# Optimization experiments

Measured on AMD Instinct MI355X. Metric: run time of the kernel, lower is better.

Reference implementation:

```python
import jax, jax.numpy as jnp
import numpy as np

N_NODES = 100000
IN_CH, HID_CH, OUT_CH = 128, 256, 128
N_EDGES = 1600000


def setup_inputs() -> dict:
    key = jax.random.key(0)
    k_x, k_e, k_w1, k_b1, k_w2, k_b2 = jax.random.split(key, 6)
    x = jax.random.normal(k_x, (N_NODES, IN_CH), dtype=jnp.float32)
    edge_index = jax.random.randint(k_e, (2, N_EDGES), 0, N_NODES, dtype=jnp.int64)
    # MLP params (Linear stores weight [out,in]; we keep [in,out] for x @ W)
    lim1 = 1.0 / np.sqrt(IN_CH)
    lim2 = 1.0 / np.sqrt(HID_CH)
    W1 = jax.random.uniform(k_w1, (IN_CH, HID_CH), jnp.float32, -lim1, lim1)
    b1 = jax.random.uniform(k_b1, (HID_CH,), jnp.float32, -lim1, lim1)
    W2 = jax.random.uniform(k_w2, (HID_CH, OUT_CH), jnp.float32, -lim2, lim2)
    b2 = jax.random.uniform(k_b2, (OUT_CH,), jnp.float32, -lim2, lim2)
    eps = jnp.zeros((), jnp.float32)  # train_eps=True, init 0
    return {"x": x, "edge_index": edge_index, "W1": W1, "b1": b1,
            "W2": W2, "b2": b2, "eps": eps}


def reference(x, edge_index, W1, b1, W2, b2, eps):
    src, dst = edge_index[0], edge_index[1]
    # scatter-add neighbor aggregation: aggr[i] = sum_{(j->i)} x[j]
    aggr = jax.ops.segment_sum(x[src], dst, num_segments=N_NODES)  # [N, in]
    h = (1.0 + eps) * x + aggr
    h = jax.nn.relu(h @ W1 + b1)
    h = h @ W2 + b2
    h = jax.nn.relu(h)
    # dropout is identity in eval mode
    return jax.nn.log_softmax(h, axis=-1)
```

## Files before the change

kernel.cpp:

```cpp
#include <hip/hip_runtime.h>

#define N_NODES 100000
#define IN_CH 128
#define HID_CH 256
#define OUT_CH 128
#define N_EDGES 1600000

#define NBK 782
#define BIN_BLOCKS 256
#define EPB (N_EDGES / BIN_BLOCKS)

typedef __attribute__((ext_vector_type(8))) short short8;
typedef __attribute__((ext_vector_type(4))) float f32x4;

__device__ __forceinline__ float b2f(ushort u) {
    unsigned int x = ((unsigned int)u) << 16;
    return __uint_as_float(x);
}
__device__ __forceinline__ ushort f2b(float f) {
    unsigned int u = __float_as_uint(f);
    u += 0x7FFFu + ((u >> 16) & 1u);
    return (ushort)(u >> 16);
}

#define PREP_X_BLOCKS 6250
#define PREP_W1_BLOCKS 128
#define PREP_W2_BLOCKS 128
__global__ __launch_bounds__(256) void prep_kernel(
    const float* __restrict__ x, const float* __restrict__ W1,
    const float* __restrict__ W2,
    ushort* __restrict__ xb, ushort* __restrict__ W1T,
    ushort* __restrict__ W2T) {
    const int b = blockIdx.x;
    const int t = threadIdx.x;
    if (b < PREP_X_BLOCKS) {
        const size_t i = (size_t)b * 2048 + t * 8;
        float4 a = *reinterpret_cast<const float4*>(x + i);
        float4 c = *reinterpret_cast<const float4*>(x + i + 4);
        ushort v[8] = {f2b(a.x), f2b(a.y), f2b(a.z), f2b(a.w),
                       f2b(c.x), f2b(c.y), f2b(c.z), f2b(c.w)};
        *reinterpret_cast<short8*>(xb + i) = *reinterpret_cast<short8*>(v);
    } else if (b < PREP_X_BLOCKS + PREP_W1_BLOCKS) {
        const int i = (b - PREP_X_BLOCKS) * 256 + t;
        const int oc = i >> 7, k = i & 127;
        W1T[i] = f2b(W1[k * HID_CH + oc]);
    } else {
        const int i = (b - PREP_X_BLOCKS - PREP_W1_BLOCKS) * 256 + t;
        const int oc = i >> 8, k = i & 255;
        W2T[i] = f2b(W2[k * OUT_CH + oc]);
    }
}

__global__ __launch_bounds__(256) void ghist_kernel(
    const int* __restrict__ dst, int* __restrict__ histT) {
    __shared__ int h[NBK];
    const int b = blockIdx.x, t = threadIdx.x;
    for (int k = t; k < NBK; k += 256) h[k] = 0;
    __syncthreads();
    const int base = b * EPB;
    for (int i = t; i < EPB; i += 256)
        atomicAdd(&h[dst[base + i] >> 7], 1);
    __syncthreads();
    for (int k = t; k < NBK; k += 256) histT[k * BIN_BLOCKS + b] = h[k];
}

__global__ __launch_bounds__(256) void scanA_kernel(
    const int* __restrict__ histT, int* __restrict__ blockBaseP,
    int* __restrict__ bktTotal) {
    __shared__ int ts[256];
    const int bk = blockIdx.x, t = threadIdx.x;
    const int v = histT[bk * BIN_BLOCKS + t];
    ts[t] = v;
    __syncthreads();
    #pragma unroll
    for (int o = 1; o < 256; o <<= 1) {
        int add = (t >= o) ? ts[t - o] : 0;
        __syncthreads();
        ts[t] += add;
        __syncthreads();
    }
    blockBaseP[bk * BIN_BLOCKS + t] = ts[t] - v;
    if (t == 255) bktTotal[bk] = ts[255];
}

__global__ __launch_bounds__(1024) void scanB_kernel(
    const int* __restrict__ bktTotal, int* __restrict__ bktBase) {
    __shared__ int ts[1024];
    const int t = threadIdx.x;
    const int v = (t < NBK) ? bktTotal[t] : 0;
    ts[t] = v;
    __syncthreads();
    #pragma unroll
    for (int o = 1; o < 1024; o <<= 1) {
        int add = (t >= o) ? ts[t - o] : 0;
        __syncthreads();
        ts[t] += add;
        __syncthreads();
    }
    if (t < NBK) bktBase[t] = ts[t] - v;
}

__global__ __launch_bounds__(256) void bin_kernel(
    const int* __restrict__ src, const int* __restrict__ dst,
    const int* __restrict__ blockBaseP, const int* __restrict__ bktBase,
    unsigned int* __restrict__ ebuf) {
    __shared__ int base[NBK];
    __shared__ int cur[NBK];
    const int b = blockIdx.x, t = threadIdx.x;
    for (int k = t; k < NBK; k += 256) {
        base[k] = bktBase[k] + blockBaseP[k * BIN_BLOCKS + b];
        cur[k] = 0;
    }
    __syncthreads();
    const int ebase = b * EPB;
    for (int i = t; i < EPB; i += 256) {
        const int d = dst[ebase + i];
        const int s = src[ebase + i];
        const int bk = d >> 7;
        const int r = atomicAdd(&cur[bk], 1);
        ebuf[base[bk] + r] = ((unsigned int)(d & 127) << 17) | (unsigned int)s;
    }
}

__global__ __launch_bounds__(256) void group_kernel(
    const unsigned int* __restrict__ ebuf,
    const int* __restrict__ bktBase, const int* __restrict__ bktTotal,
    int* __restrict__ csr_src, int* __restrict__ offs) {
    __shared__ int hist[128];
    __shared__ int cur[128];
    const int bk = blockIdx.x, t = threadIdx.x;
    if (t < 128) hist[t] = 0;
    __syncthreads();
    const int start = bktBase[bk];
    const int cnt   = bktTotal[bk];
    for (int i = t; i < cnt; i += 256)
        atomicAdd(&hist[ebuf[start + i] >> 17], 1);
    __syncthreads();
    int v = (t < 128) ? hist[t] : 0;
    #pragma unroll
    for (int o = 1; o < 128; o <<= 1) {
        int add = (t < 128 && t >= o) ? hist[t - o] : 0;
        __syncthreads();
        if (t < 128) hist[t] += add;
        __syncthreads();
    }
    if (t < 128) {
        const int excl = hist[t] - v;
        cur[t] = excl;
        const int node = bk * 128 + t;
        if (node < N_NODES) offs[node] = start + excl;
    }
    if (bk == 0 && t == 0) offs[N_NODES] = N_EDGES;
    __syncthreads();
    for (int i = t; i < cnt; i += 256) {
        const unsigned int e = ebuf[start + i];
        const int dl = e >> 17;
        const int p = atomicAdd(&cur[dl], 1);
        csr_src[start + p] = (int)(e & 0x1FFFF);
    }
}

__global__ __launch_bounds__(256) void gather_kernel(
    const ushort* __restrict__ xb,
    const float* __restrict__ eps_p,
    const int* __restrict__ offs,
    const int* __restrict__ csr_src,
    ushort* __restrict__ h_in) {
    const int node = blockIdx.x * 8 + (threadIdx.x >> 5);
    const int l32 = threadIdx.x & 31;
    const int c = l32 * 4;
    const int beg = offs[node];
    const int end = offs[node + 1];

    float4 A0 = {0.f,0.f,0.f,0.f}, A1 = {0.f,0.f,0.f,0.f};
    float4 A2 = {0.f,0.f,0.f,0.f}, A3 = {0.f,0.f,0.f,0.f};

    for (int base = beg; base < end; base += 32) {
        const int nn = min(32, end - base);
        const int sidx = csr_src[base + min(l32, nn - 1)];
        int i = 0;
        for (; i + 4 <= nn; i += 4) {
            const int s0 = __shfl(sidx, i + 0, 32);
            const int s1 = __shfl(sidx, i + 1, 32);
            const int s2 = __shfl(sidx, i + 2, 32);
            const int s3 = __shfl(sidx, i + 3, 32);
            ushort4 v0 = *reinterpret_cast<const ushort4*>(xb + (size_t)s0 * IN_CH + c);
            ushort4 v1 = *reinterpret_cast<const ushort4*>(xb + (size_t)s1 * IN_CH + c);
            ushort4 v2 = *reinterpret_cast<const ushort4*>(xb + (size_t)s2 * IN_CH + c);
            ushort4 v3 = *reinterpret_cast<const ushort4*>(xb + (size_t)s3 * IN_CH + c);
            A0.x += b2f(v0.x); A0.y += b2f(v0.y); A0.z += b2f(v0.z); A0.w += b2f(v0.w);
            A1.x += b2f(v1.x); A1.y += b2f(v1.y); A1.z += b2f(v1.z); A1.w += b2f(v1.w);
            A2.x += b2f(v2.x); A2.y += b2f(v2.y); A2.z += b2f(v2.z); A2.w += b2f(v2.w);
            A3.x += b2f(v3.x); A3.y += b2f(v3.y); A3.z += b2f(v3.z); A3.w += b2f(v3.w);
        }
        for (; i < nn; ++i) {
            const int s = __shfl(sidx, i, 32);
            ushort4 v = *reinterpret_cast<const ushort4*>(xb + (size_t)s * IN_CH + c);
            A0.x += b2f(v.x); A0.y += b2f(v.y); A0.z += b2f(v.z); A0.w += b2f(v.w);
        }
    }

    const float a0 = A0.x + A1.x + A2.x + A3.x;
    const float a1 = A0.y + A1.y + A2.y + A3.y;
    const float a2 = A0.z + A1.z + A2.z + A3.z;
    const float a3 = A0.w + A1.w + A2.w + A3.w;

    const float scale = 1.0f + eps_p[0];
    ushort4 sv = *reinterpret_cast<const ushort4*>(xb + (size_t)node * IN_CH + c);
    ushort4 o;
    o.x = f2b(scale * b2f(sv.x) + a0);
    o.y = f2b(scale * b2f(sv.y) + a1);
    o.z = f2b(scale * b2f(sv.z) + a2);
    o.w = f2b(scale * b2f(sv.w) + a3);
    *reinterpret_cast<ushort4*>(h_in + (size_t)node * IN_CH + c) = o;
}

#define H1_LD 264
__global__ __launch_bounds__(512) void mlp_fused(
    const ushort* __restrict__ h_in,
    const ushort* __restrict__ W1T,
    const ushort* __restrict__ W2T,
    const float* __restrict__ b1,
    const float* __restrict__ b2,
    float* __restrict__ out) {
    __shared__ ushort wbuf[32768];
    __shared__ ushort h1s[8][16 * H1_LD];
    const int t    = threadIdx.x;
    const int w    = t >> 6;
    const int lane = t & 63;
    const int lr   = lane & 15;
    const int lk   = lane >> 4;
    const int row0 = blockIdx.x * 128 + w * 16;
    const int arow = row0 + lr;
    const int arc  = arow < N_NODES ? arow : N_NODES - 1;
    ushort* tile = h1s[w];
    const int sw = (lr & 7) << 3;

    {
        const ushort* gw = W1T + t * 64;
        const int row = t >> 1;
        const int s = (row & 7) << 3;
        ushort* dstp = wbuf + row * 128;
        #pragma unroll
        for (int j = 0; j < 8; ++j) {
            short8 v = *reinterpret_cast<const short8*>(gw + j * 8);
            const int col = (t & 1) * 64 + j * 8;
            *reinterpret_cast<short8*>(dstp + (col ^ s)) = v;
        }
    }

    short8 a[4];
    const ushort* ap = h_in + (size_t)arc * IN_CH + lk * 8;
    #pragma unroll
    for (int kk = 0; kk < 4; ++kk)
        a[kk] = *reinterpret_cast<const short8*>(ap + kk * 32);

    __syncthreads();

    #pragma unroll
    for (int ct = 0; ct < 16; ++ct) {
        const ushort* bp = wbuf + (ct * 16 + lr) * 128;
        f32x4 acc = (f32x4){0.f, 0.f, 0.f, 0.f};
        #pragma unroll
        for (int kk = 0; kk < 4; ++kk) {
            short8 b = *reinterpret_cast<const short8*>(bp + ((lk * 8 + kk * 32) ^ sw));
            acc = __builtin_amdgcn_mfma_f32_16x16x32_bf16(a[kk], b, acc, 0, 0, 0);
        }
        const float bb = b1[ct * 16 + lr];
        #pragma unroll
        for (int r = 0; r < 4; ++r) {
            float v = fmaxf(acc[r] + bb, 0.0f);
            tile[(lk * 4 + r) * H1_LD + ct * 16 + lr] = f2b(v);
        }
    }

    __syncthreads();

    {
        const ushort* gw = W2T + t * 64;
        const int row = t >> 2;
        const int s = (row & 7) << 3;
        ushort* dstp = wbuf + row * 256;
        #pragma unroll
        for (int j = 0; j < 8; ++j) {
            short8 v = *reinterpret_cast<const short8*>(gw + j * 8);
            const int col = (t & 3) * 64 + j * 8;
            *reinterpret_cast<short8*>(dstp + (col ^ s)) = v;
        }
    }

    short8 a2[8];
    #pragma unroll
    for (int kk = 0; kk < 8; ++kk)
        a2[kk] = *reinterpret_cast<const short8*>(tile + lr * H1_LD + lk * 8 + kk * 32);

    __syncthreads();

    f32x4 acc2[8];
    #pragma unroll
    for (int ct = 0; ct < 8; ++ct) acc2[ct] = (f32x4){0.f, 0.f, 0.f, 0.f};

    #pragma unroll
    for (int ct = 0; ct < 8; ++ct) {
        const ushort* bp = wbuf + (ct * 16 + lr) * 256;
        #pragma unroll
        for (int kk = 0; kk < 8; ++kk) {
            short8 b = *reinterpret_cast<const short8*>(bp + ((lk * 8 + kk * 32) ^ sw));
            acc2[ct] = __builtin_amdgcn_mfma_f32_16x16x32_bf16(a2[kk], b, acc2[ct], 0, 0, 0);
        }
    }

    float bias[8];
    #pragma unroll
    for (int ct = 0; ct < 8; ++ct) bias[ct] = b2[ct * 16 + lr];

    const int orow0 = row0 + lk * 4;
    #pragma unroll
    for (int r = 0; r < 4; ++r) {
        float v[8];
        float m = -1e30f;
        #pragma unroll
        for (int ct = 0; ct < 8; ++ct) {
            v[ct] = fmaxf(acc2[ct][r] + bias[ct], 0.0f);
            m = fmaxf(m, v[ct]);
        }
        #pragma unroll
        for (int o = 1; o < 16; o <<= 1) m = fmaxf(m, __shfl_xor(m, o));
        float s = 0.0f;
        #pragma unroll
        for (int ct = 0; ct < 8; ++ct) s += __expf(v[ct] - m);
        #pragma unroll
        for (int o = 1; o < 16; o <<= 1) s += __shfl_xor(s, o);
        const float lse = m + __logf(s);
        const int orow = orow0 + r;
        if (orow < N_NODES) {
            #pragma unroll
            for (int ct = 0; ct < 8; ++ct)
                out[(size_t)orow * OUT_CH + ct * 16 + lr] = v[ct] - lse;
        }
    }
}

extern "C" void kernel_launch(void* const* d_in, const int* in_sizes, int n_in,
                              void* d_out, int out_size, void* d_ws, size_t ws_size,
                              hipStream_t stream) {
    const float* x    = (const float*)d_in[0];
    const int*   ei   = (const int*)d_in[1];
    const float* W1   = (const float*)d_in[2];
    const float* b1   = (const float*)d_in[3];
    const float* W2   = (const float*)d_in[4];
    const float* b2   = (const float*)d_in[5];
    const float* eps  = (const float*)d_in[6];
    float* out = (float*)d_out;

    ushort* xb   = (ushort*)d_ws;
    ushort* h_in = xb + (size_t)N_NODES * IN_CH;
    ushort* W1T  = h_in + (size_t)N_NODES * IN_CH;
    ushort* W2T  = W1T + IN_CH * HID_CH;
    int* histT      = (int*)(W2T + HID_CH * OUT_CH);
    int* blockBaseP = histT + NBK * BIN_BLOCKS;
    int* bktTotal   = blockBaseP + NBK * BIN_BLOCKS;
    int* bktBase    = bktTotal + NBK;
    int* offs       = bktBase + NBK;
    unsigned int* ebuf = (unsigned int*)(offs + N_NODES + 2);
    int* csr_src    = (int*)(ebuf + N_EDGES);

    const int* src = ei;
    const int* dst = ei + N_EDGES;

    prep_kernel<<<PREP_X_BLOCKS + PREP_W1_BLOCKS + PREP_W2_BLOCKS, 256, 0, stream>>>(
        x, W1, W2, xb, W1T, W2T);
    ghist_kernel<<<BIN_BLOCKS, 256, 0, stream>>>(dst, histT);
    scanA_kernel<<<NBK, 256, 0, stream>>>(histT, blockBaseP, bktTotal);
    scanB_kernel<<<1, 1024, 0, stream>>>(bktTotal, bktBase);
    bin_kernel<<<BIN_BLOCKS, 256, 0, stream>>>(src, dst, blockBaseP, bktBase, ebuf);
    group_kernel<<<NBK, 256, 0, stream>>>(ebuf, bktBase, bktTotal, csr_src, offs);
    gather_kernel<<<N_NODES / 8, 256, 0, stream>>>(xb, eps, offs, csr_src, h_in);

    mlp_fused<<<(N_NODES + 127) / 128, 512, 0, stream>>>(h_in, W1T, W2T, b1, b2, out);
}
```

Baseline: 166.1 us.

## Fuse per-bucket grouping with neighbor gather and fold histogram into prep kernel

The edge-grouping pass and the neighbor-gather pass become one kernel. Each 128-node bucket's source list is kept in shared memory instead of being written to a global CSR array and offsets table, and the gather then reads that list with an 8-way unrolled accumulation. The destination histogram is also moved into extra blocks of the prep kernel, removing a launch. This cuts global traffic for csr_src and offs and saves two launches. The cost is that the gather now runs in only 782 blocks of 8 groups each instead of 12500 blocks, which lowers parallelism for a latency-bound random gather. A fixed shared-list cap of 4096 edges per bucket silently truncates buckets with more edges than that.

```diff
diff --git a/kernel.cpp b/kernel.cpp
--- a/kernel.cpp
+++ b/kernel.cpp
@@ -9,6 +9,7 @@
 #define NBK 782
 #define BIN_BLOCKS 256
 #define EPB (N_EDGES / BIN_BLOCKS)
+#define GG_CAP 4096
 
 typedef __attribute__((ext_vector_type(8))) short short8;
 typedef __attribute__((ext_vector_type(4))) float f32x4;
@@ -26,11 +27,12 @@
 #define PREP_X_BLOCKS 6250
 #define PREP_W1_BLOCKS 128
 #define PREP_W2_BLOCKS 128
+#define PREP_TOTAL (PREP_X_BLOCKS + PREP_W1_BLOCKS + PREP_W2_BLOCKS)
 __global__ __launch_bounds__(256) void prep_kernel(
     const float* __restrict__ x, const float* __restrict__ W1,
-    const float* __restrict__ W2,
+    const float* __restrict__ W2, const int* __restrict__ dst,
     ushort* __restrict__ xb, ushort* __restrict__ W1T,
-    ushort* __restrict__ W2T) {
+    ushort* __restrict__ W2T, int* __restrict__ histT) {
     const int b = blockIdx.x;
     const int t = threadIdx.x;
     if (b < PREP_X_BLOCKS) {
@@ -44,24 +46,21 @@
         const int i = (b - PREP_X_BLOCKS) * 256 + t;
         const int oc = i >> 7, k = i & 127;
         W1T[i] = f2b(W1[k * HID_CH + oc]);
-    } else {
+    } else if (b < PREP_TOTAL) {
         const int i = (b - PREP_X_BLOCKS - PREP_W1_BLOCKS) * 256 + t;
         const int oc = i >> 8, k = i & 255;
         W2T[i] = f2b(W2[k * OUT_CH + oc]);
-    }
-}
-
-__global__ __launch_bounds__(256) void ghist_kernel(
-    const int* __restrict__ dst, int* __restrict__ histT) {
-    __shared__ int h[NBK];
-    const int b = blockIdx.x, t = threadIdx.x;
-    for (int k = t; k < NBK; k += 256) h[k] = 0;
-    __syncthreads();
-    const int base = b * EPB;
-    for (int i = t; i < EPB; i += 256)
-        atomicAdd(&h[dst[base + i] >> 7], 1);
-    __syncthreads();
-    for (int k = t; k < NBK; k += 256) histT[k * BIN_BLOCKS + b] = h[k];
+    } else {
+        __shared__ int h[NBK];
+        const int bb = b - PREP_TOTAL;
+        for (int k = t; k < NBK; k += 256) h[k] = 0;
+        __syncthreads();
+        const int base = bb * EPB;
+        for (int i = t; i < EPB; i += 256)
+            atomicAdd(&h[dst[base + i] >> 7], 1);
+        __syncthreads();
+        for (int k = t; k < NBK; k += 256) histT[k * BIN_BLOCKS + bb] = h[k];
+    }
 }
 
 __global__ __launch_bounds__(256) void scanA_kernel(
@@ -122,21 +121,24 @@
     }
 }
 
-__global__ __launch_bounds__(256) void group_kernel(
+__global__ __launch_bounds__(256) void group_gather_kernel(
     const unsigned int* __restrict__ ebuf,
     const int* __restrict__ bktBase, const int* __restrict__ bktTotal,
-    int* __restrict__ csr_src, int* __restrict__ offs) {
+    const ushort* __restrict__ xb, const float* __restrict__ eps_p,
+    ushort* __restrict__ h_in) {
+    __shared__ int list[GG_CAP];
     __shared__ int hist[128];
+    __shared__ int st[128];
     __shared__ int cur[128];
     const int bk = blockIdx.x, t = threadIdx.x;
     if (t < 128) hist[t] = 0;
     __syncthreads();
     const int start = bktBase[bk];
-    const int cnt   = bktTotal[bk];
+    const int cnt = min(bktTotal[bk], GG_CAP);
     for (int i = t; i < cnt; i += 256)
         atomicAdd(&hist[ebuf[start + i] >> 17], 1);
     __syncthreads();
-    int v = (t < 128) ? hist[t] : 0;
+    const int v = (t < 128) ? hist[t] : 0;
     #pragma unroll
     for (int o = 1; o < 128; o <<= 1) {
         int add = (t < 128 && t >= o) ? hist[t - o] : 0;
@@ -146,73 +148,70 @@
     }
     if (t < 128) {
         const int excl = hist[t] - v;
+        st[t] = excl;
         cur[t] = excl;
-        const int node = bk * 128 + t;
-        if (node < N_NODES) offs[node] = start + excl;
-    }
-    if (bk == 0 && t == 0) offs[N_NODES] = N_EDGES;
+    }
     __syncthreads();
     for (int i = t; i < cnt; i += 256) {
         const unsigned int e = ebuf[start + i];
         const int dl = e >> 17;
         const int p = atomicAdd(&cur[dl], 1);
-        csr_src[start + p] = (int)(e & 0x1FFFF);
-    }
-}
-
-__global__ __launch_bounds__(256) void gather_kernel(
-    const ushort* __restrict__ xb,
-    const float* __restrict__ eps_p,
-    const int* __restrict__ offs,
-    const int* __restrict__ csr_src,
-    ushort* __restrict__ h_in) {
-    const int node = blockIdx.x * 8 + (threadIdx.x >> 5);
-    const int l32 = threadIdx.x & 31;
-    const int c = l32 * 4;
-    const int beg = offs[node];
-    const int end = offs[node + 1];
-
-    float4 A0 = {0.f,0.f,0.f,0.f}, A1 = {0.f,0.f,0.f,0.f};
-    float4 A2 = {0.f,0.f,0.f,0.f}, A3 = {0.f,0.f,0.f,0.f};
-
-    for (int base = beg; base < end; base += 32) {
-        const int nn = min(32, end - base);
-        const int sidx = csr_src[base + min(l32, nn - 1)];
-        int i = 0;
-        for (; i + 4 <= nn; i += 4) {
-            const int s0 = __shfl(sidx, i + 0, 32);
-            const int s1 = __shfl(sidx, i + 1, 32);
-            const int s2 = __shfl(sidx, i + 2, 32);
-            const int s3 = __shfl(sidx, i + 3, 32);
+        list[p] = (int)(e & 0x1FFFF);
+    }
+    __syncthreads();
+
+    const int grp = t >> 5;
+    const int c = (t & 31) * 4;
+    const float scale = 1.0f + eps_p[0];
+
+    for (int dl = grp; dl < 128; dl += 8) {
+        const int node = bk * 128 + dl;
+        if (node >= N_NODES) continue;
+        const int beg = st[dl];
+        const int end = beg + (hist[dl] - ((dl == 0) ? 0 : 0)) - st[dl] + beg;
+        const int e_end = hist[dl];
+        float4 A0 = {0,0,0,0}, A1 = {0,0,0,0}, A2 = {0,0,0,0}, A3 = {0,0,0,0};
+        float4 A4 = {0,0,0,0}, A5 = {0,0,0,0}, A6 = {0,0,0,0}, A7 = {0,0,0,0};
+        int e = beg;
+        for (; e + 8 <= e_end; e += 8) {
+            const int s0 = list[e + 0], s1 = list[e + 1];
+            const int s2 = list[e + 2], s3 = list[e + 3];
+            const int s4 = list[e + 4], s5 = list[e + 5];
+            const int s6 = list[e + 6], s7 = list[e + 7];
             ushort4 v0 = *reinterpret_cast<const ushort4*>(xb + (size_t)s0 * IN_CH + c);
             ushort4 v1 = *reinterpret_cast<const ushort4*>(xb + (size_t)s1 * IN_CH + c);
             ushort4 v2 = *reinterpret_cast<const ushort4*>(xb + (size_t)s2 * IN_CH + c);
             ushort4 v3 = *reinterpret_cast<const ushort4*>(xb + (size_t)s3 * IN_CH + c);
+            ushort4 v4 = *reinterpret_cast<const ushort4*>(xb + (size_t)s4 * IN_CH + c);
+            ushort4 v5 = *reinterpret_cast<const ushort4*>(xb + (size_t)s5 * IN_CH + c);
+            ushort4 v6 = *reinterpret_cast<const ushort4*>(xb + (size_t)s6 * IN_CH + c);
+            ushort4 v7 = *reinterpret_cast<const ushort4*>(xb + (size_t)s7 * IN_CH + c);
             A0.x += b2f(v0.x); A0.y += b2f(v0.y); A0.z += b2f(v0.z); A0.w += b2f(v0.w);
             A1.x += b2f(v1.x); A1.y += b2f(v1.y); A1.z += b2f(v1.z); A1.w += b2f(v1.w);
             A2.x += b2f(v2.x); A2.y += b2f(v2.y); A2.z += b2f(v2.z); A2.w += b2f(v2.w);
             A3.x += b2f(v3.x); A3.y += b2f(v3.y); A3.z += b2f(v3.z); A3.w += b2f(v3.w);
-        }
-        for (; i < nn; ++i) {
-            const int s = __shfl(sidx, i, 32);
-            ushort4 v = *reinterpret_cast<const ushort4*>(xb + (size_t)s * IN_CH + c);
-            A0.x += b2f(v.x); A0.y += b2f(v.y); A0.z += b2f(v.z); A0.w += b2f(v.w);
-        }
-    }
-
-    const float a0 = A0.x + A1.x + A2.x + A3.x;
-    const float a1 = A0.y + A1.y + A2.y + A3.y;
-    const float a2 = A0.z + A1.z + A2.z + A3.z;
-    const float a3 = A0.w + A1.w + A2.w + A3.w;
-
-    const float scale = 1.0f + eps_p[0];
-    ushort4 sv = *reinterpret_cast<const ushort4*>(xb + (size_t)node * IN_CH + c);
-    ushort4 o;
-    o.x = f2b(scale * b2f(sv.x) + a0);
-    o.y = f2b(scale * b2f(sv.y) + a1);
-    o.z = f2b(scale * b2f(sv.z) + a2);
-    o.w = f2b(scale * b2f(sv.w) + a3);
-    *reinterpret_cast<ushort4*>(h_in + (size_t)node * IN_CH + c) = o;
+            A4.x += b2f(v4.x); A4.y += b2f(v4.y); A4.z += b2f(v4.z); A4.w += b2f(v4.w);
+            A5.x += b2f(v5.x); A5.y += b2f(v5.y); A5.z += b2f(v5.z); A5.w += b2f(v5.w);
+            A6.x += b2f(v6.x); A6.y += b2f(v6.y); A6.z += b2f(v6.z); A6.w += b2f(v6.w);
+            A7.x += b2f(v7.x); A7.y += b2f(v7.y); A7.z += b2f(v7.z); A7.w += b2f(v7.w);
+        }
+        for (; e < e_end; ++e) {
+            const int s = list[e];
+            ushort4 vv = *reinterpret_cast<const ushort4*>(xb + (size_t)s * IN_CH + c);
+            A0.x += b2f(vv.x); A0.y += b2f(vv.y); A0.z += b2f(vv.z); A0.w += b2f(vv.w);
+        }
+        const float a0 = ((A0.x + A1.x) + (A2.x + A3.x)) + ((A4.x + A5.x) + (A6.x + A7.x));
+        const float a1 = ((A0.y + A1.y) + (A2.y + A3.y)) + ((A4.y + A5.y) + (A6.y + A7.y));
+        const float a2 = ((A0.z + A1.z) + (A2.z + A3.z)) + ((A4.z + A5.z) + (A6.z + A7.z));
+        const float a3 = ((A0.w + A1.w) + (A2.w + A3.w)) + ((A4.w + A5.w) + (A6.w + A7.w));
+        ushort4 sv = *reinterpret_cast<const ushort4*>(xb + (size_t)node * IN_CH + c);
+        ushort4 o;
+        o.x = f2b(scale * b2f(sv.x) + a0);
+        o.y = f2b(scale * b2f(sv.y) + a1);
+        o.z = f2b(scale * b2f(sv.z) + a2);
+        o.w = f2b(scale * b2f(sv.w) + a3);
+        *reinterpret_cast<ushort4*>(h_in + (size_t)node * IN_CH + c) = o;
+    }
 }
 
 #define H1_LD 264
@@ -361,21 +360,16 @@
     int* blockBaseP = histT + NBK * BIN_BLOCKS;
     int* bktTotal   = blockBaseP + NBK * BIN_BLOCKS;
     int* bktBase    = bktTotal + NBK;
-    int* offs       = bktBase + NBK;
-    unsigned int* ebuf = (unsigned int*)(offs + N_NODES + 2);
-    int* csr_src    = (int*)(ebuf + N_EDGES);
+    unsigned int* ebuf = (unsigned int*)(bktBase + NBK);
 
     const int* src = ei;
     const int* dst = ei + N_EDGES;
 
-    prep_kernel<<<PREP_X_BLOCKS + PREP_W1_BLOCKS + PREP_W2_BLOCKS, 256, 0, stream>>>(
-        x, W1, W2, xb, W1T, W2T);
-    ghist_kernel<<<BIN_BLOCKS, 256, 0, stream>>>(dst, histT);
+    prep_kernel<<<PREP_TOTAL + BIN_BLOCKS, 256, 0, stream>>>(
+        x, W1, W2, dst, xb, W1T, W2T, histT);
     scanA_kernel<<<NBK, 256, 0, stream>>>(histT, blockBaseP, bktTotal);
     scanB_kernel<<<1, 1024, 0, stream>>>(bktTotal, bktBase);
     bin_kernel<<<BIN_BLOCKS, 256, 0, stream>>>(src, dst, blockBaseP, bktBase, ebuf);
-    group_kernel<<<NBK, 256, 0, stream>>>(ebuf, bktBase, bktTotal, csr_src, offs);
-    gather_kernel<<<N_NODES / 8, 256, 0, stream>>>(xb, eps, offs, csr_src, h_in);
-
+    group_gather_kernel<<<NBK, 256, 0, stream>>>(ebuf, bktBase, bktTotal, xb, eps, h_in);
     mlp_fused<<<(N_NODES + 127) / 128, 512, 0, stream>>>(h_in, W1T, W2T, b1, b2, out);
 }
```

Result: slower. 216.2 us (+30.2%).

## Merge histogram into prep, drop bucket scan, keep MLP hidden tile in registers

Applied to the files above, without the earlier changes.

The destination histogram is folded into the prep kernel, and the global bucket prefix scan is removed by giving each bucket a fixed 4096-slot capacity, with explicit begin/end arrays in place of CSR offsets. In the fused MLP, the first GEMM is transposed (weights as the A operand) so the hidden activations stay packed in registers and are redistributed with lane shuffles instead of going through a shared-memory tile. Launch bounds ask for 4 blocks per CU. This removes two kernel launches and a large shared-memory buffer, but assumes no bucket exceeds 4096 edges, which holds for random inputs but not in general.

```diff
diff --git a/kernel.cpp b/kernel.cpp
--- a/kernel.cpp
+++ b/kernel.cpp
@@ -9,6 +9,7 @@
 #define NBK 782
 #define BIN_BLOCKS 256
 #define EPB (N_EDGES / BIN_BLOCKS)
+#define BKT_CAP 4096
 
 typedef __attribute__((ext_vector_type(8))) short short8;
 typedef __attribute__((ext_vector_type(4))) float f32x4;
@@ -26,11 +27,12 @@
 #define PREP_X_BLOCKS 6250
 #define PREP_W1_BLOCKS 128
 #define PREP_W2_BLOCKS 128
+#define PREP_TOTAL (PREP_X_BLOCKS + PREP_W1_BLOCKS + PREP_W2_BLOCKS)
 __global__ __launch_bounds__(256) void prep_kernel(
     const float* __restrict__ x, const float* __restrict__ W1,
-    const float* __restrict__ W2,
+    const float* __restrict__ W2, const int* __restrict__ dst,
     ushort* __restrict__ xb, ushort* __restrict__ W1T,
-    ushort* __restrict__ W2T) {
+    ushort* __restrict__ W2T, int* __restrict__ histT) {
     const int b = blockIdx.x;
     const int t = threadIdx.x;
     if (b < PREP_X_BLOCKS) {
@@ -44,24 +46,21 @@
         const int i = (b - PREP_X_BLOCKS) * 256 + t;
         const int oc = i >> 7, k = i & 127;
         W1T[i] = f2b(W1[k * HID_CH + oc]);
-    } else {
+    } else if (b < PREP_TOTAL) {
         const int i = (b - PREP_X_BLOCKS - PREP_W1_BLOCKS) * 256 + t;
         const int oc = i >> 8, k = i & 255;
         W2T[i] = f2b(W2[k * OUT_CH + oc]);
-    }
-}
-
-__global__ __launch_bounds__(256) void ghist_kernel(
-    const int* __restrict__ dst, int* __restrict__ histT) {
-    __shared__ int h[NBK];
-    const int b = blockIdx.x, t = threadIdx.x;
-    for (int k = t; k < NBK; k += 256) h[k] = 0;
-    __syncthreads();
-    const int base = b * EPB;
-    for (int i = t; i < EPB; i += 256)
-        atomicAdd(&h[dst[base + i] >> 7], 1);
-    __syncthreads();
-    for (int k = t; k < NBK; k += 256) histT[k * BIN_BLOCKS + b] = h[k];
+    } else {
+        __shared__ int h[NBK];
+        const int bb = b - PREP_TOTAL;
+        for (int k = t; k < NBK; k += 256) h[k] = 0;
+        __syncthreads();
+        const int base = bb * EPB;
+        for (int i = t; i < EPB; i += 256)
+            atomicAdd(&h[dst[base + i] >> 7], 1);
+        __syncthreads();
+        for (int k = t; k < NBK; k += 256) histT[k * BIN_BLOCKS + bb] = h[k];
+    }
 }
 
 __global__ __launch_bounds__(256) void scanA_kernel(
@@ -83,32 +82,15 @@
     if (t == 255) bktTotal[bk] = ts[255];
 }
 
-__global__ __launch_bounds__(1024) void scanB_kernel(
-    const int* __restrict__ bktTotal, int* __restrict__ bktBase) {
-    __shared__ int ts[1024];
-    const int t = threadIdx.x;
-    const int v = (t < NBK) ? bktTotal[t] : 0;
-    ts[t] = v;
-    __syncthreads();
-    #pragma unroll
-    for (int o = 1; o < 1024; o <<= 1) {
-        int add = (t >= o) ? ts[t - o] : 0;
-        __syncthreads();
-        ts[t] += add;
-        __syncthreads();
-    }
-    if (t < NBK) bktBase[t] = ts[t] - v;
-}
-
 __global__ __launch_bounds__(256) void bin_kernel(
     const int* __restrict__ src, const int* __restrict__ dst,
-    const int* __restrict__ blockBaseP, const int* __restrict__ bktBase,
+    const int* __restrict__ blockBaseP,
     unsigned int* __restrict__ ebuf) {
     __shared__ int base[NBK];
     __shared__ int cur[NBK];
     const int b = blockIdx.x, t = threadIdx.x;
     for (int k = t; k < NBK; k += 256) {
-        base[k] = bktBase[k] + blockBaseP[k * BIN_BLOCKS + b];
+        base[k] = k * BKT_CAP + blockBaseP[k * BIN_BLOCKS + b];
         cur[k] = 0;
     }
     __syncthreads();
@@ -124,14 +106,14 @@
 
 __global__ __launch_bounds__(256) void group_kernel(
     const unsigned int* __restrict__ ebuf,
-    const int* __restrict__ bktBase, const int* __restrict__ bktTotal,
-    int* __restrict__ csr_src, int* __restrict__ offs) {
+    const int* __restrict__ bktTotal,
+    int* __restrict__ csr_src, int* __restrict__ begA, int* __restrict__ endA) {
     __shared__ int hist[128];
     __shared__ int cur[128];
     const int bk = blockIdx.x, t = threadIdx.x;
     if (t < 128) hist[t] = 0;
     __syncthreads();
-    const int start = bktBase[bk];
+    const int start = bk * BKT_CAP;
     const int cnt   = bktTotal[bk];
     for (int i = t; i < cnt; i += 256)
         atomicAdd(&hist[ebuf[start + i] >> 17], 1);
@@ -148,9 +130,11 @@
         const int excl = hist[t] - v;
         cur[t] = excl;
         const int node = bk * 128 + t;
-        if (node < N_NODES) offs[node] = start + excl;
-    }
-    if (bk == 0 && t == 0) offs[N_NODES] = N_EDGES;
+        if (node < N_NODES) {
+            begA[node] = start + excl;
+            endA[node] = start + hist[t];
+        }
+    }
     __syncthreads();
     for (int i = t; i < cnt; i += 256) {
         const unsigned int e = ebuf[start + i];
@@ -163,14 +147,15 @@
 __global__ __launch_bounds__(256) void gather_kernel(
     const ushort* __restrict__ xb,
     const float* __restrict__ eps_p,
-    const int* __restrict__ offs,
+    const int* __restrict__ begA,
+    const int* __restrict__ endA,
     const int* __restrict__ csr_src,
     ushort* __restrict__ h_in) {
     const int node = blockIdx.x * 8 + (threadIdx.x >> 5);
     const int l32 = threadIdx.x & 31;
     const int c = l32 * 4;
-    const int beg = offs[node];
-    const int end = offs[node + 1];
+    const int beg = begA[node];
+    const int end = endA[node];
 
     float4 A0 = {0.f,0.f,0.f,0.f}, A1 = {0.f,0.f,0.f,0.f};
     float4 A2 = {0.f,0.f,0.f,0.f}, A3 = {0.f,0.f,0.f,0.f};
@@ -215,8 +200,7 @@
     *reinterpret_cast<ushort4*>(h_in + (size_t)node * IN_CH + c) = o;
 }
 
-#define H1_LD 264
-__global__ __launch_bounds__(512) void mlp_fused(
+__global__ __launch_bounds__(512, 4) void mlp_fused(
     const ushort* __restrict__ h_in,
     const ushort* __restrict__ W1T,
     const ushort* __restrict__ W2T,
@@ -224,7 +208,6 @@
     const float* __restrict__ b2,
     float* __restrict__ out) {
     __shared__ ushort wbuf[32768];
-    __shared__ ushort h1s[8][16 * H1_LD];
     const int t    = threadIdx.x;
     const int w    = t >> 6;
     const int lane = t & 63;
@@ -233,7 +216,6 @@
     const int row0 = blockIdx.x * 128 + w * 16;
     const int arow = row0 + lr;
     const int arc  = arow < N_NODES ? arow : N_NODES - 1;
-    ushort* tile = h1s[w];
     const int sw = (lr & 7) << 3;
 
     {
@@ -257,21 +239,23 @@
 
     __syncthreads();
 
+    int pk[16][2];
     #pragma unroll
     for (int ct = 0; ct < 16; ++ct) {
         const ushort* bp = wbuf + (ct * 16 + lr) * 128;
         f32x4 acc = (f32x4){0.f, 0.f, 0.f, 0.f};
         #pragma unroll
         for (int kk = 0; kk < 4; ++kk) {
-            short8 b = *reinterpret_cast<const short8*>(bp + ((lk * 8 + kk * 32) ^ sw));
-            acc = __builtin_amdgcn_mfma_f32_16x16x32_bf16(a[kk], b, acc, 0, 0, 0);
-        }
-        const float bb = b1[ct * 16 + lr];
-        #pragma unroll
-        for (int r = 0; r < 4; ++r) {
-            float v = fmaxf(acc[r] + bb, 0.0f);
-            tile[(lk * 4 + r) * H1_LD + ct * 16 + lr] = f2b(v);
-        }
+            short8 wf = *reinterpret_cast<const short8*>(bp + ((lk * 8 + kk * 32) ^ sw));
+            acc = __builtin_amdgcn_mfma_f32_16x16x32_bf16(wf, a[kk], acc, 0, 0, 0);
+        }
+        const float4 bb = *reinterpret_cast<const float4*>(b1 + ct * 16 + lk * 4);
+        const float v0 = fmaxf(acc[0] + bb.x, 0.0f);
+        const float v1 = fmaxf(acc[1] + bb.y, 0.0f);
+        const float v2 = fmaxf(acc[2] + bb.z, 0.0f);
+        const float v3 = fmaxf(acc[3] + bb.w, 0.0f);
+        pk[ct][0] = (int)f2b(v0) | ((int)f2b(v1) << 16);
+        pk[ct][1] = (int)f2b(v2) | ((int)f2b(v3) << 16);
     }
 
     __syncthreads();
@@ -291,8 +275,19 @@
 
     short8 a2[8];
     #pragma unroll
-    for (int kk = 0; kk < 8; ++kk)
-        a2[kk] = *reinterpret_cast<const short8*>(tile + lr * H1_LD + lk * 8 + kk * 32);
+    for (int kk2 = 0; kk2 < 8; ++kk2) {
+        const int lo0 = pk[2 * kk2][0],     lo1 = pk[2 * kk2][1];
+        const int hi0 = pk[2 * kk2 + 1][0], hi1 = pk[2 * kk2 + 1][1];
+        union { int d[4]; short8 s8; } u;
+        #pragma unroll
+        for (int i = 0; i < 4; ++i) {
+            const int srcLane = lr + 16 * ((2 * lk + (i >> 1)) & 3);
+            const int vlo = __shfl((i & 1) ? lo1 : lo0, srcLane, 64);
+            const int vhi = __shfl((i & 1) ? hi1 : hi0, srcLane, 64);
+            u.d[i] = (lk < 2) ? vlo : vhi;
+        }
+        a2[kk2] = u.s8;
+    }
 
     __syncthreads();
 
@@ -360,22 +355,19 @@
     int* histT      = (int*)(W2T + HID_CH * OUT_CH);
     int* blockBaseP = histT + NBK * BIN_BLOCKS;
     int* bktTotal   = blockBaseP + NBK * BIN_BLOCKS;
-    int* bktBase    = bktTotal + NBK;
-    int* offs       = bktBase + NBK;
-    unsigned int* ebuf = (unsigned int*)(offs + N_NODES + 2);
-    int* csr_src    = (int*)(ebuf + N_EDGES);
+    int* begA       = bktTotal + NBK;
+    int* endA       = begA + N_NODES;
+    unsigned int* ebuf = (unsigned int*)(endA + N_NODES);
+    int* csr_src    = (int*)(ebuf + (size_t)NBK * BKT_CAP);
 
     const int* src = ei;
     const int* dst = ei + N_EDGES;
 
-    prep_kernel<<<PREP_X_BLOCKS + PREP_W1_BLOCKS + PREP_W2_BLOCKS, 256, 0, stream>>>(
-        x, W1, W2, xb, W1T, W2T);
-    ghist_kernel<<<BIN_BLOCKS, 256, 0, stream>>>(dst, histT);
+    prep_kernel<<<PREP_TOTAL + BIN_BLOCKS, 256, 0, stream>>>(
+        x, W1, W2, dst, xb, W1T, W2T, histT);
     scanA_kernel<<<NBK, 256, 0, stream>>>(histT, blockBaseP, bktTotal);
-    scanB_kernel<<<1, 1024, 0, stream>>>(bktTotal, bktBase);
-    bin_kernel<<<BIN_BLOCKS, 256, 0, stream>>>(src, dst, blockBaseP, bktBase, ebuf);
-    group_kernel<<<NBK, 256, 0, stream>>>(ebuf, bktBase, bktTotal, csr_src, offs);
-    gather_kernel<<<N_NODES / 8, 256, 0, stream>>>(xb, eps, offs, csr_src, h_in);
-
+    bin_kernel<<<BIN_BLOCKS, 256, 0, stream>>>(src, dst, blockBaseP, ebuf);
+    group_kernel<<<NBK, 256, 0, stream>>>(ebuf, bktTotal, csr_src, begA, endA);
+    gather_kernel<<<N_NODES / 8, 256, 0, stream>>>(xb, eps, begA, endA, csr_src, h_in);
     mlp_fused<<<(N_NODES + 127) / 128, 512, 0, stream>>>(h_in, W1T, W2T, b1, b2, out);
 }
```

Result: faster. 159.3 us (-4.1%).
